# Performance work log

Measured on AMD Instinct MI355X. Metric: run time of the kernel, lower is better.

## Reference

```python
import jax, jax.numpy as jnp
import numpy as np


def setup_inputs() -> dict:
    key = jax.random.key(0)
    ks = jax.random.split(key, 16)
    B, T, A, R, M, D = 128, 1024, 512, 1024, 256, 256  # batch, max_time, annot, rnn, memory, attn dims
    F, K = 32, 31  # location filters, kernel size
    s = jnp.float32(0.02)
    return dict(
        memory=jax.random.normal(ks[0], (B, M), jnp.float32),
        context=jax.random.normal(ks[1], (B, A), jnp.float32),
        rnn_state=jax.random.normal(ks[2], (B, R), jnp.float32),
        annots=jax.random.normal(ks[3], (B, T, A), jnp.float32),
        atten=jax.random.uniform(ks[4], (B, 2, T), jnp.float32),
        mask=jax.random.randint(ks[5], (B, T), 0, 2).astype(jnp.int32),
        Wi=jax.random.normal(ks[6], (3 * R, A + M), jnp.float32) * s,   # GRU input weights (r,z,n)
        Wh=jax.random.normal(ks[7], (3 * R, R), jnp.float32) * s,       # GRU hidden weights
        bi=jnp.zeros((3 * R,), jnp.float32),
        bh=jnp.zeros((3 * R,), jnp.float32),
        conv_w=jax.random.normal(ks[8], (F, 2, K), jnp.float32) * s,    # loc_conv (OIH)
        loc_w=jax.random.normal(ks[9], (D, F), jnp.float32) * s,
        loc_b=jnp.zeros((D,), jnp.float32),
        q_w=jax.random.normal(ks[10], (D, R), jnp.float32) * s,
        q_b=jnp.zeros((D,), jnp.float32),
        a_w=jax.random.normal(ks[11], (D, A), jnp.float32) * s,
        a_b=jnp.zeros((D,), jnp.float32),
        v_w=jax.random.normal(ks[12], (1, D), jnp.float32) * s,
    )


def reference(memory, context, rnn_state, annots, atten, mask,
              Wi, Wh, bi, bh, conv_w, loc_w, loc_b, q_w, q_b, a_w, a_b, v_w):
    # --- GRUCell (torch gate order: r, z, n) ---
    x = jnp.concatenate([memory, context], axis=-1)          # (B, M+A)
    gi = x @ Wi.T + bi                                        # (B, 3R)
    gh = rnn_state @ Wh.T + bh                                # (B, 3R)
    ir, iz, inn = jnp.split(gi, 3, axis=-1)
    hr, hz, hn = jnp.split(gh, 3, axis=-1)
    r = jax.nn.sigmoid(ir + hr)
    z = jax.nn.sigmoid(iz + hz)
    n = jnp.tanh(inn + r * hn)
    h = (1.0 - z) * n + z * rnn_state                         # (B, R) rnn_output

    # --- Location-sensitive attention ---
    pad = (conv_w.shape[-1] - 1) // 2
    loc = jax.lax.conv_general_dilated(atten, conv_w, (1,), [(pad, pad)],
                                       dimension_numbers=('NCH', 'OIH', 'NCH'))  # (B, F, T)
    ploc = jnp.einsum('bft,df->btd', loc, loc_w) + loc_b      # (B, T, D)
    pq = (h @ q_w.T + q_b)[:, None, :]                        # (B, 1, D)
    pa = jnp.einsum('bta,da->btd', annots, a_w) + a_b         # (B, T, D)
    align = jnp.einsum('btd,d->bt', jnp.tanh(pq + pa + ploc), v_w[0])  # (B, T)

    # masked softmax (mask==0 -> -inf)
    align = jnp.where(mask != 0, align, jnp.float32(-1e30))
    align = jax.nn.softmax(align, axis=-1)

    # context = bmm(align, annots)
    ctx = jnp.einsum('bt,bta->ba', align, annots)             # (B, A)
    return (h, ctx, align)
```

## Files before the change

### kernel.cpp

```cpp
#include <hip/hip_runtime.h>
#include <cstddef>

constexpr int B  = 128;
constexpr int T  = 1024;
constexpr int AD = 512;
constexpr int R  = 1024;
constexpr int M  = 256;
constexpr int DD = 256;
constexpr int F  = 32;
constexpr int KW = 31;
constexpr int PADW = 15;
constexpr int XDIM = M + AD;
constexpr int G3 = 3 * R;
constexpr size_t BG3 = (size_t)B * G3;

using short8 = __attribute__((ext_vector_type(8))) short;
using f32x4  = __attribute__((ext_vector_type(4))) float;

__device__ __forceinline__ float sigmoidf(float x) { return 1.f / (1.f + __expf(-x)); }

__device__ __forceinline__ unsigned short f2bf(float x) {
  unsigned int u = __float_as_uint(x);
  u += 0x7FFFu + ((u >> 16) & 1u);
  return (unsigned short)(u >> 16);
}

__device__ __forceinline__ float tanh_fast(float x) {
  float e = __expf(2.f * x);
  return 1.f - 2.f / (e + 1.f);
}

__device__ __forceinline__ uint4 pack_bf8(float4 f0, float4 f1) {
  uint4 r;
  r.x = f2bf(f0.x) | ((unsigned)f2bf(f0.y) << 16);
  r.y = f2bf(f0.z) | ((unsigned)f2bf(f0.w) << 16);
  r.z = f2bf(f1.x) | ((unsigned)f2bf(f1.y) << 16);
  r.w = f2bf(f1.z) | ((unsigned)f2bf(f1.w) << 16);
  return r;
}

__device__ __forceinline__ void load_lds16(const void* g, void* l) {
  __builtin_amdgcn_global_load_lds(
      (const __attribute__((address_space(1))) unsigned int*)g,
      (__attribute__((address_space(3))) unsigned int*)l, 16, 0, 0);
}

__global__ __launch_bounds__(256) void prep_wsw(const float* __restrict__ aw,
                                                const float* __restrict__ lw,
                                                unsigned short* __restrict__ awsw,
                                                unsigned short* __restrict__ lwsw) {
  int idx = blockIdx.x * 256 + threadIdx.x;
  int chunk = idx >> 10;
  int rn = (idx & 1023) >> 2;
  int u = idx & 3;
  int su = u ^ ((rn >> 1) & 3);
  const float* src;
  unsigned short* dst;
  if (chunk < 16) {
    src = aw + (size_t)rn * AD + chunk * 32 + u * 8;
    dst = awsw + chunk * 8192 + rn * 32 + su * 8;
  } else {
    src = lw + (size_t)rn * F + u * 8;
    dst = lwsw + rn * 32 + su * 8;
  }
  float4 f0 = *(const float4*)src;
  float4 f1 = *(const float4*)(src + 4);
  *(uint4*)dst = pack_bf8(f0, f1);
}

__global__ __launch_bounds__(256) void prep_gru(const float* __restrict__ mem,
                                                const float* __restrict__ ctxin,
                                                const float* __restrict__ rnn,
                                                const float* __restrict__ Wi,
                                                const float* __restrict__ Wh,
                                                unsigned short* __restrict__ Wib,
                                                unsigned short* __restrict__ Whb,
                                                unsigned short* __restrict__ xb,
                                                unsigned short* __restrict__ rnnb) {
  const int t = blockIdx.x * 256 + threadIdx.x;
  const float* src;
  unsigned short* dst;
  if (t < 294912) {
    src = Wi + (size_t)t * 8;
    dst = Wib + (size_t)t * 8;
  } else if (t < 688128) {
    size_t e = (size_t)(t - 294912) * 8;
    src = Wh + e;
    dst = Whb + e;
  } else if (t < 700416) {
    size_t e = (size_t)(t - 688128) * 8;
    int row = (int)(e / XDIM), col = (int)(e % XDIM);
    src = (col < M) ? (mem + (size_t)row * M + col)
                    : (ctxin + (size_t)row * AD + (col - M));
    dst = xb + e;
  } else {
    size_t e = (size_t)(t - 700416) * 8;
    src = rnn + e;
    dst = rnnb + e;
  }
  float4 f0 = *(const float4*)src;
  float4 f1 = *(const float4*)(src + 4);
  *(uint4*)dst = pack_bf8(f0, f1);
}

__global__ __launch_bounds__(256) void loc_conv(const float* __restrict__ atten,
                                                const float* __restrict__ conv_w,
                                                unsigned short* __restrict__ locw) {
  __shared__ float s_att[2 * 94];
  __shared__ float s_cw[F * 62];
  const int tid = threadIdx.x;
  const int t0 = blockIdx.x * 64, b = blockIdx.y;
  for (int i = tid; i < 2 * 94; i += 256) {
    int c = i / 94, ii = i - c * 94;
    int gt = t0 - PADW + ii;
    s_att[i] = (gt >= 0 && gt < T) ? atten[((size_t)b * 2 + c) * T + gt] : 0.f;
  }
  for (int i = tid; i < F * 62; i += 256) s_cw[i] = conv_w[i];
  __syncthreads();
  const int f = tid & 31;
  const int tb = (tid >> 5) * 8;
  float a8[8] = {0.f, 0.f, 0.f, 0.f, 0.f, 0.f, 0.f, 0.f};
#pragma unroll
  for (int c = 0; c < 2; ++c) {
    float win[38];
#pragma unroll
    for (int i = 0; i < 38; ++i) win[i] = s_att[c * 94 + tb + i];
#pragma unroll
    for (int k = 0; k < KW; ++k) {
      float w = s_cw[f * 62 + c * 31 + k];
#pragma unroll
      for (int ti = 0; ti < 8; ++ti) a8[ti] += w * win[ti + k];
    }
  }
#pragma unroll
  for (int ti = 0; ti < 8; ++ti)
    locw[((size_t)b * T + t0 + tb + ti) * F + f] = f2bf(a8[ti]);
}

__global__ __launch_bounds__(256, 2) void gemm_gru(const unsigned short* __restrict__ xb,
                                                   const unsigned short* __restrict__ rnnb,
                                                   const unsigned short* __restrict__ Wib,
                                                   const unsigned short* __restrict__ Whb,
                                                   float* __restrict__ outp) {
  const int tid = threadIdx.x;
  const int wv = tid >> 6, lane = tid & 63;
  const int lm = lane & 15, lg = lane >> 4;
  const int g0 = blockIdx.x * 64;
  const int z = blockIdx.y;
  const int which = z >> 2, q = z & 3;
  const unsigned short* __restrict__ A = which ? rnnb : xb;
  const unsigned short* __restrict__ W = which ? Whb : Wib;
  const int K = which ? R : XDIM;
  const int Kq = K >> 2;
  const int nch = Kq >> 5;
  float* __restrict__ C = outp + (size_t)z * BG3;

  const unsigned short* aA = A + (size_t)(wv * 32 + lm) * K + q * Kq + lg * 8;
  const unsigned short* bW = W + (size_t)(g0 + lm) * K + q * Kq + lg * 8;

  f32x4 acc[2][4];
#pragma unroll
  for (int i = 0; i < 2; ++i)
#pragma unroll
    for (int j = 0; j < 4; ++j) acc[i][j] = (f32x4){0.f, 0.f, 0.f, 0.f};

#pragma unroll 2
  for (int ch = 0; ch < nch; ++ch) {
    const int k = ch * 32;
    short8 a8[2], b8[4];
#pragma unroll
    for (int i = 0; i < 2; ++i)
      a8[i] = *(const short8*)(aA + (size_t)i * 16 * K + k);
#pragma unroll
    for (int j = 0; j < 4; ++j)
      b8[j] = *(const short8*)(bW + (size_t)j * 16 * K + k);
#pragma unroll
    for (int j = 0; j < 4; ++j)
#pragma unroll
      for (int i = 0; i < 2; ++i)
        acc[i][j] = __builtin_amdgcn_mfma_f32_16x16x32_bf16(a8[i], b8[j], acc[i][j], 0, 0, 0);
  }

#pragma unroll
  for (int i = 0; i < 2; ++i)
#pragma unroll
    for (int reg = 0; reg < 4; ++reg) {
      const size_t row = (size_t)(wv * 32 + i * 16 + lg * 4 + reg) * G3 + g0 + lm;
#pragma unroll
      for (int j = 0; j < 4; ++j) C[row + j * 16] = acc[i][j][reg];
    }
}

__global__ __launch_bounds__(256) void gru_combine(const float* __restrict__ gp,
                                                   const float* __restrict__ bi,
                                                   const float* __restrict__ bh,
                                                   const float* __restrict__ hprev,
                                                   float* __restrict__ hout) {
  int idx = blockIdx.x * 256 + threadIdx.x;
  int b = idx >> 10, j = idx & (R - 1);
  float ir = bi[j], iz = bi[R + j], inn = bi[2 * R + j];
  float hr = bh[j], hz = bh[R + j], hn = bh[2 * R + j];
#pragma unroll
  for (int z = 0; z < 4; ++z) {
    const float* g = gp + (size_t)z * BG3 + (size_t)b * G3;
    ir += g[j]; iz += g[R + j]; inn += g[2 * R + j];
  }
#pragma unroll
  for (int z = 4; z < 8; ++z) {
    const float* g = gp + (size_t)z * BG3 + (size_t)b * G3;
    hr += g[j]; hz += g[R + j]; hn += g[2 * R + j];
  }
  float r = sigmoidf(ir + hr);
  float z = sigmoidf(iz + hz);
  float n = tanhf(inn + r * hn);
  float hp = hprev[(size_t)b * R + j];
  hout[(size_t)b * R + j] = (1.f - z) * n + z * hp;
}

__global__ __launch_bounds__(256) void pq_kernel(const float* __restrict__ h,
                                                 const float* __restrict__ q_w,
                                                 const float* __restrict__ q_b,
                                                 float* __restrict__ pq) {
  __shared__ __align__(16) float sh[R];
  int b = blockIdx.x, tid = threadIdx.x;
  ((float4*)sh)[tid] = ((const float4*)(h + (size_t)b * R))[tid];
  __syncthreads();
  const float* wr = q_w + (size_t)tid * R;
  float acc = 0.f;
#pragma unroll 4
  for (int k = 0; k < R; k += 4) {
    float4 w = *(const float4*)&wr[k];
    float4 x = *(const float4*)&sh[k];
    acc += w.x * x.x + w.y * x.y + w.z * x.z + w.w * x.w;
  }
  pq[(size_t)b * DD + tid] = acc + q_b[tid];
}

__global__ __launch_bounds__(512, 4) void attn_fused(
    const float* __restrict__ annots, const unsigned short* __restrict__ locw,
    const int* __restrict__ mask,
    const unsigned short* __restrict__ awsw, const unsigned short* __restrict__ lwsw,
    const float* __restrict__ loc_b, const float* __restrict__ a_b,
    const float* __restrict__ v_w, const float* __restrict__ pq,
    float* __restrict__ u_out, float* __restrict__ ctx_part,
    float* __restrict__ S_part) {
  __shared__ __align__(16) unsigned short s_A[2][128 * 32];
  __shared__ __align__(16) unsigned short s_B[2][256 * 32];

  const int tid = threadIdx.x;
  const int wv = tid >> 6, lane = tid & 63;
  const int lm = lane & 15, lg = lane >> 4;
  const int wr = wv >> 2, wc = wv & 3;
  const int g = blockIdx.x, b = blockIdx.y;
  const int t0 = g * 128;
  const int ar = tid >> 2, au = tid & 3;
  const int asu = au ^ ((ar >> 1) & 3);
  const int sufb = lg ^ ((lm >> 1) & 3);

  const float* arow = annots + ((size_t)b * T + t0 + ar) * AD + au * 8;

  {
    float4 f0 = *(const float4*)(arow);
    float4 f1 = *(const float4*)(arow + 4);
    load_lds16(awsw + wv * 1024 + lane * 8, &s_B[0][wv * 1024]);
    load_lds16(awsw + wv * 1024 + 512 + lane * 8, &s_B[0][wv * 1024 + 512]);
    *(uint4*)&s_A[0][ar * 32 + asu * 8] = pack_bf8(f0, f1);
  }
  float4 aN0 = *(const float4*)(arow + 32);
  float4 aN1 = *(const float4*)(arow + 36);
  uint4 lvN = {0, 0, 0, 0};

  f32x4 acc[4][4];
#pragma unroll
  for (int j = 0; j < 4; ++j) {
    int d = wc * 64 + j * 16 + lm;
    float base = pq[(size_t)b * DD + d] + a_b[d] + loc_b[d];
    f32x4 bv = {base, base, base, base};
#pragma unroll
    for (int i = 0; i < 4; ++i) acc[i][j] = bv;
  }
  __syncthreads();

#pragma unroll 1
  for (int ks = 0; ks <= 16; ++ks) {
    const int cur = ks & 1, nxt = cur ^ 1;
    if (ks + 1 <= 16) {
      const unsigned short* img = (ks + 1 < 16) ? (awsw + (ks + 1) * 8192) : lwsw;
      load_lds16(img + wv * 1024 + lane * 8, &s_B[nxt][wv * 1024]);
      load_lds16(img + wv * 1024 + 512 + lane * 8, &s_B[nxt][wv * 1024 + 512]);
    }
    float4 aN20, aN21;
    uint4 lvN2;
    if (ks + 2 <= 15) {
      aN20 = *(const float4*)(arow + (ks + 2) * 32);
      aN21 = *(const float4*)(arow + (ks + 2) * 32 + 4);
    } else if (ks + 2 == 16) {
      lvN2 = *(const uint4*)(locw + ((size_t)b * T + t0 + ar) * F + au * 8);
    }
    if (ks + 1 <= 15) {
      *(uint4*)&s_A[nxt][ar * 32 + asu * 8] = pack_bf8(aN0, aN1);
    } else if (ks + 1 == 16) {
      *(uint4*)&s_A[nxt][ar * 32 + asu * 8] = lvN;
    }
    short8 afr[4], bfr[4];
#pragma unroll
    for (int i = 0; i < 4; ++i)
      afr[i] = *(const short8*)&s_A[cur][(wr * 64 + i * 16 + lm) * 32 + sufb * 8];
#pragma unroll
    for (int j = 0; j < 4; ++j)
      bfr[j] = *(const short8*)&s_B[cur][(wc * 64 + j * 16 + lm) * 32 + sufb * 8];
#pragma unroll
    for (int j = 0; j < 4; ++j)
#pragma unroll
      for (int i = 0; i < 4; ++i)
        acc[i][j] = __builtin_amdgcn_mfma_f32_16x16x32_bf16(afr[i], bfr[j], acc[i][j], 0, 0, 0);
    if (ks <= 13) {
      asm volatile("s_waitcnt vmcnt(2) lgkmcnt(0)" ::: "memory");
    } else if (ks == 14) {
      asm volatile("s_waitcnt vmcnt(1) lgkmcnt(0)" ::: "memory");
    } else {
      asm volatile("s_waitcnt vmcnt(0) lgkmcnt(0)" ::: "memory");
    }
    __builtin_amdgcn_s_barrier();
    if (ks + 2 <= 15) { aN0 = aN20; aN1 = aN21; }
    else if (ks + 2 == 16) lvN = lvN2;
  }

  float* s_e = (float*)s_A;
  float* s_u = s_e + 512;
  float* s_red = s_e + 644;
  float vwv[4];
#pragma unroll
  for (int j = 0; j < 4; ++j) vwv[j] = v_w[wc * 64 + j * 16 + lm];
#pragma unroll
  for (int i = 0; i < 4; ++i) {
#pragma unroll
    for (int reg = 0; reg < 4; ++reg) {
      float p = 0.f;
#pragma unroll
      for (int j = 0; j < 4; ++j) p += vwv[j] * tanh_fast(acc[i][j][reg]);
      p += __shfl_xor(p, 1);
      p += __shfl_xor(p, 2);
      p += __shfl_xor(p, 4);
      p += __shfl_xor(p, 8);
      if (lm == 0) s_e[wc * 128 + wr * 64 + i * 16 + lg * 4 + reg] = p;
    }
  }
  __syncthreads();
  if (tid < 128) {
    float e = s_e[tid] + s_e[128 + tid] + s_e[256 + tid] + s_e[384 + tid];
    bool mk = mask[(size_t)b * T + t0 + tid] != 0;
    float u = mk ? __expf(e) : 0.f;
    u_out[(size_t)b * T + t0 + tid] = u;
    s_u[tid] = u;
    float p = u;
    p += __shfl_xor(p, 1);
    p += __shfl_xor(p, 2);
    p += __shfl_xor(p, 4);
    p += __shfl_xor(p, 8);
    p += __shfl_xor(p, 16);
    p += __shfl_xor(p, 32);
    if (lane == 0) s_red[tid >> 6] = p;
  }
  __syncthreads();
  if (tid == 0) S_part[b * 8 + g] = s_red[0] + s_red[1];
  {
    const float* ap = annots + ((size_t)b * T + t0) * AD + tid;
    float c0 = 0.f, c1 = 0.f, c2 = 0.f, c3 = 0.f;
#pragma unroll 2
    for (int t = 0; t < 128; t += 4) {
      c0 += s_u[t + 0] * ap[(size_t)(t + 0) * AD];
      c1 += s_u[t + 1] * ap[(size_t)(t + 1) * AD];
      c2 += s_u[t + 2] * ap[(size_t)(t + 2) * AD];
      c3 += s_u[t + 3] * ap[(size_t)(t + 3) * AD];
    }
    ctx_part[(size_t)g * ((size_t)B * AD) + (size_t)b * AD + tid] = (c0 + c1) + (c2 + c3);
  }
}

__global__ __launch_bounds__(512) void finalize(const float* __restrict__ S_part,
                                                const float* __restrict__ ctx_part,
                                                float* __restrict__ al,
                                                float* __restrict__ ctxo) {
  int b = blockIdx.x, tid = threadIdx.x;
  float S = 0.f;
#pragma unroll
  for (int g = 0; g < 8; ++g) S += S_part[b * 8 + g];
  float inv = 1.f / S;
  float2* ap = (float2*)(al + (size_t)b * T);
  float2 v = ap[tid];
  v.x *= inv; v.y *= inv;
  ap[tid] = v;
  float c = 0.f;
#pragma unroll
  for (int p = 0; p < 8; ++p)
    c += ctx_part[(size_t)p * ((size_t)B * AD) + (size_t)b * AD + tid];
  ctxo[(size_t)b * AD + tid] = c * inv;
}

extern "C" void kernel_launch(void* const* d_in, const int* in_sizes, int n_in,
                              void* d_out, int out_size, void* d_ws, size_t ws_size,
                              hipStream_t stream) {
  const float* memory = (const float*)d_in[0];
  const float* context = (const float*)d_in[1];
  const float* rnn = (const float*)d_in[2];
  const float* annots = (const float*)d_in[3];
  const float* atten = (const float*)d_in[4];
  const int* mask = (const int*)d_in[5];
  const float* Wi = (const float*)d_in[6];
  const float* Wh = (const float*)d_in[7];
  const float* bi = (const float*)d_in[8];
  const float* bh = (const float*)d_in[9];
  const float* conv_w = (const float*)d_in[10];
  const float* loc_w = (const float*)d_in[11];
  const float* loc_b = (const float*)d_in[12];
  const float* q_w = (const float*)d_in[13];
  const float* q_b = (const float*)d_in[14];
  const float* a_w = (const float*)d_in[15];
  const float* a_b = (const float*)d_in[16];
  const float* v_w = (const float*)d_in[17];

  float* out = (float*)d_out;
  float* out_h = out;
  float* out_ctx = out + (size_t)B * R;
  float* out_al = out_ctx + (size_t)B * AD;

  float* ws = (float*)d_ws;
  float* gp_ws = ws;
  float* pq_ws = gp_ws + 8 * BG3;
  float* S_part = pq_ws + (size_t)B * DD;
  float* ctx_part = S_part + (size_t)B * 8;
  unsigned short* awsw = (unsigned short*)(ctx_part + (size_t)8 * B * AD);
  unsigned short* lwsw = awsw + (size_t)16 * 8192;
  unsigned short* locw = lwsw + 8192;
  unsigned short* Wib = locw + (size_t)B * T * F;
  unsigned short* Whb = Wib + (size_t)G3 * XDIM;
  unsigned short* xb = Whb + (size_t)G3 * R;
  unsigned short* rnnb = xb + (size_t)B * XDIM;

  prep_wsw<<<68, 256, 0, stream>>>(a_w, loc_w, awsw, lwsw);
  prep_gru<<<2800, 256, 0, stream>>>(memory, context, rnn, Wi, Wh,
                                     Wib, Whb, xb, rnnb);
  loc_conv<<<dim3(T / 64, B), 256, 0, stream>>>(atten, conv_w, locw);
  gemm_gru<<<dim3(48, 8), 256, 0, stream>>>(xb, rnnb, Wib, Whb, gp_ws);
  gru_combine<<<(B * R) / 256, 256, 0, stream>>>(gp_ws, bi, bh, rnn, out_h);
  pq_kernel<<<B, 256, 0, stream>>>(out_h, q_w, q_b, pq_ws);
  attn_fused<<<dim3(8, B), 512, 0, stream>>>(annots, locw, mask, awsw, lwsw,
                                             loc_b, a_b, v_w, pq_ws,
                                             out_al, ctx_part, S_part);
  finalize<<<B, 512, 0, stream>>>(S_part, ctx_part, out_al, out_ctx);
}
```

Baseline: 185.0 us.

## Halve attention tile to 64 timesteps with 256-thread blocks and 16 partials

Shrinks the fused attention kernel's time tile from 128 to 64 rows, using 4 waves per block and doubling the grid to 16 time groups per batch. Each wave now covers a 64-wide slice of the D dimension for all 64 rows, and each thread loads four B-chunks per stage instead of two. The context reduction reads float2 per thread, and finalize sums 16 partials. The aim is more blocks and better occupancy or latency hiding. The cost is that the a_w weight tiles are streamed twice as often per timestep and the partial buffers double in size.

```diff
diff --git a/kernel.cpp b/kernel.cpp
--- a/kernel.cpp
+++ b/kernel.cpp
@@ -236,7 +236,7 @@
   pq[(size_t)b * DD + tid] = acc + q_b[tid];
 }
 
-__global__ __launch_bounds__(512, 4) void attn_fused(
+__global__ __launch_bounds__(256, 4) void attn_fused(
     const float* __restrict__ annots, const unsigned short* __restrict__ locw,
     const int* __restrict__ mask,
     const unsigned short* __restrict__ awsw, const unsigned short* __restrict__ lwsw,
@@ -244,15 +244,14 @@
     const float* __restrict__ v_w, const float* __restrict__ pq,
     float* __restrict__ u_out, float* __restrict__ ctx_part,
     float* __restrict__ S_part) {
-  __shared__ __align__(16) unsigned short s_A[2][128 * 32];
+  __shared__ __align__(16) unsigned short s_A[2][64 * 32];
   __shared__ __align__(16) unsigned short s_B[2][256 * 32];
 
   const int tid = threadIdx.x;
   const int wv = tid >> 6, lane = tid & 63;
   const int lm = lane & 15, lg = lane >> 4;
-  const int wr = wv >> 2, wc = wv & 3;
   const int g = blockIdx.x, b = blockIdx.y;
-  const int t0 = g * 128;
+  const int t0 = g * 64;
   const int ar = tid >> 2, au = tid & 3;
   const int asu = au ^ ((ar >> 1) & 3);
   const int sufb = lg ^ ((lm >> 1) & 3);
@@ -262,8 +261,9 @@
   {
     float4 f0 = *(const float4*)(arow);
     float4 f1 = *(const float4*)(arow + 4);
-    load_lds16(awsw + wv * 1024 + lane * 8, &s_B[0][wv * 1024]);
-    load_lds16(awsw + wv * 1024 + 512 + lane * 8, &s_B[0][wv * 1024 + 512]);
+#pragma unroll
+    for (int kq = 0; kq < 4; ++kq)
+      load_lds16(awsw + wv * 2048 + kq * 512 + lane * 8, &s_B[0][wv * 2048 + kq * 512]);
     *(uint4*)&s_A[0][ar * 32 + asu * 8] = pack_bf8(f0, f1);
   }
   float4 aN0 = *(const float4*)(arow + 32);
@@ -273,21 +273,24 @@
   f32x4 acc[4][4];
 #pragma unroll
   for (int j = 0; j < 4; ++j) {
-    int d = wc * 64 + j * 16 + lm;
+    int d = wv * 64 + j * 16 + lm;
     float base = pq[(size_t)b * DD + d] + a_b[d] + loc_b[d];
     f32x4 bv = {base, base, base, base};
 #pragma unroll
     for (int i = 0; i < 4; ++i) acc[i][j] = bv;
   }
-  __syncthreads();
+  asm volatile("s_waitcnt vmcnt(2) lgkmcnt(0)" ::: "memory");
+  __builtin_amdgcn_s_barrier();
 
 #pragma unroll 1
   for (int ks = 0; ks <= 16; ++ks) {
     const int cur = ks & 1, nxt = cur ^ 1;
     if (ks + 1 <= 16) {
       const unsigned short* img = (ks + 1 < 16) ? (awsw + (ks + 1) * 8192) : lwsw;
-      load_lds16(img + wv * 1024 + lane * 8, &s_B[nxt][wv * 1024]);
-      load_lds16(img + wv * 1024 + 512 + lane * 8, &s_B[nxt][wv * 1024 + 512]);
+#pragma unroll
+      for (int kq = 0; kq < 4; ++kq)
+        load_lds16(img + wv * 2048 + kq * 512 + lane * 8,
+                   &s_B[nxt][wv * 2048 + kq * 512]);
     }
     float4 aN20, aN21;
     uint4 lvN2;
@@ -305,10 +308,10 @@
     short8 afr[4], bfr[4];
 #pragma unroll
     for (int i = 0; i < 4; ++i)
-      afr[i] = *(const short8*)&s_A[cur][(wr * 64 + i * 16 + lm) * 32 + sufb * 8];
+      afr[i] = *(const short8*)&s_A[cur][(i * 16 + lm) * 32 + sufb * 8];
 #pragma unroll
     for (int j = 0; j < 4; ++j)
-      bfr[j] = *(const short8*)&s_B[cur][(wc * 64 + j * 16 + lm) * 32 + sufb * 8];
+      bfr[j] = *(const short8*)&s_B[cur][(wv * 64 + j * 16 + lm) * 32 + sufb * 8];
 #pragma unroll
     for (int j = 0; j < 4; ++j)
 #pragma unroll
@@ -327,11 +330,10 @@
   }
 
   float* s_e = (float*)s_A;
-  float* s_u = s_e + 512;
-  float* s_red = s_e + 644;
+  float* s_u = s_e + 256;
   float vwv[4];
 #pragma unroll
-  for (int j = 0; j < 4; ++j) vwv[j] = v_w[wc * 64 + j * 16 + lm];
+  for (int j = 0; j < 4; ++j) vwv[j] = v_w[wv * 64 + j * 16 + lm];
 #pragma unroll
   for (int i = 0; i < 4; ++i) {
 #pragma unroll
@@ -343,12 +345,12 @@
       p += __shfl_xor(p, 2);
       p += __shfl_xor(p, 4);
       p += __shfl_xor(p, 8);
-      if (lm == 0) s_e[wc * 128 + wr * 64 + i * 16 + lg * 4 + reg] = p;
+      if (lm == 0) s_e[wv * 64 + i * 16 + lg * 4 + reg] = p;
     }
   }
   __syncthreads();
-  if (tid < 128) {
-    float e = s_e[tid] + s_e[128 + tid] + s_e[256 + tid] + s_e[384 + tid];
+  if (tid < 64) {
+    float e = s_e[tid] + s_e[64 + tid] + s_e[128 + tid] + s_e[192 + tid];
     bool mk = mask[(size_t)b * T + t0 + tid] != 0;
     float u = mk ? __expf(e) : 0.f;
     u_out[(size_t)b * T + t0 + tid] = u;
@@ -360,21 +362,23 @@
     p += __shfl_xor(p, 8);
     p += __shfl_xor(p, 16);
     p += __shfl_xor(p, 32);
-    if (lane == 0) s_red[tid >> 6] = p;
+    if (tid == 0) S_part[b * 16 + g] = p;
   }
   __syncthreads();
-  if (tid == 0) S_part[b * 8 + g] = s_red[0] + s_red[1];
   {
-    const float* ap = annots + ((size_t)b * T + t0) * AD + tid;
-    float c0 = 0.f, c1 = 0.f, c2 = 0.f, c3 = 0.f;
-#pragma unroll 2
-    for (int t = 0; t < 128; t += 4) {
-      c0 += s_u[t + 0] * ap[(size_t)(t + 0) * AD];
-      c1 += s_u[t + 1] * ap[(size_t)(t + 1) * AD];
-      c2 += s_u[t + 2] * ap[(size_t)(t + 2) * AD];
-      c3 += s_u[t + 3] * ap[(size_t)(t + 3) * AD];
-    }
-    ctx_part[(size_t)g * ((size_t)B * AD) + (size_t)b * AD + tid] = (c0 + c1) + (c2 + c3);
+    const int a0 = tid * 2;
+    const float* ap = annots + ((size_t)b * T + t0) * AD + a0;
+    float c0 = 0.f, c1 = 0.f;
+#pragma unroll 4
+    for (int t = 0; t < 64; ++t) {
+      float2 v = *(const float2*)(ap + (size_t)t * AD);
+      float w = s_u[t];
+      c0 += w * v.x;
+      c1 += w * v.y;
+    }
+    float* dst = ctx_part + (size_t)g * ((size_t)B * AD) + (size_t)b * AD + a0;
+    dst[0] = c0;
+    dst[1] = c1;
   }
 }
 
@@ -385,7 +389,7 @@
   int b = blockIdx.x, tid = threadIdx.x;
   float S = 0.f;
 #pragma unroll
-  for (int g = 0; g < 8; ++g) S += S_part[b * 8 + g];
+  for (int g = 0; g < 16; ++g) S += S_part[b * 16 + g];
   float inv = 1.f / S;
   float2* ap = (float2*)(al + (size_t)b * T);
   float2 v = ap[tid];
@@ -393,7 +397,7 @@
   ap[tid] = v;
   float c = 0.f;
 #pragma unroll
-  for (int p = 0; p < 8; ++p)
+  for (int p = 0; p < 16; ++p)
     c += ctx_part[(size_t)p * ((size_t)B * AD) + (size_t)b * AD + tid];
   ctxo[(size_t)b * AD + tid] = c * inv;
 }
@@ -429,8 +433,8 @@
   float* gp_ws = ws;
   float* pq_ws = gp_ws + 8 * BG3;
   float* S_part = pq_ws + (size_t)B * DD;
-  float* ctx_part = S_part + (size_t)B * 8;
-  unsigned short* awsw = (unsigned short*)(ctx_part + (size_t)8 * B * AD);
+  float* ctx_part = S_part + (size_t)B * 16;
+  unsigned short* awsw = (unsigned short*)(ctx_part + (size_t)16 * B * AD);
   unsigned short* lwsw = awsw + (size_t)16 * 8192;
   unsigned short* locw = lwsw + 8192;
   unsigned short* Wib = locw + (size_t)B * T * F;
@@ -445,8 +449,8 @@
   gemm_gru<<<dim3(48, 8), 256, 0, stream>>>(xb, rnnb, Wib, Whb, gp_ws);
   gru_combine<<<(B * R) / 256, 256, 0, stream>>>(gp_ws, bi, bh, rnn, out_h);
   pq_kernel<<<B, 256, 0, stream>>>(out_h, q_w, q_b, pq_ws);
-  attn_fused<<<dim3(8, B), 512, 0, stream>>>(annots, locw, mask, awsw, lwsw,
-                                             loc_b, a_b, v_w, pq_ws,
-                                             out_al, ctx_part, S_part);
+  attn_fused<<<dim3(16, B), 256, 0, stream>>>(annots, locw, mask, awsw, lwsw,
+                                              loc_b, a_b, v_w, pq_ws,
+                                              out_al, ctx_part, S_part);
   finalize<<<B, 512, 0, stream>>>(S_part, ctx_part, out_al, out_ctx);
 }
```

New measurement: 187.5 us. Within noise of the previous version (+1.4%).
